# Kernel optimization log

Measured on AMD Instinct MI355X. Metric: run time of the kernel, lower is better.

The kernel has to match this reference:

```python
import jax, jax.numpy as jnp
import numpy as np
import math

N_NODES = 100000
N_EDGES = 1600000
CUTOFF = 6.0          # max_radius
NUM_RBF = 128         # ExpNormalSmearing num_rbf
GAUSS_MIN, GAUSS_MAX, GAUSS_NB = 0.0, 10.0, 32  # GaussianExpansion(0, 10, 32)


def setup_inputs() -> dict:
    key = jax.random.key(0)
    k1, k2 = jax.random.split(key)
    pos = jax.random.normal(k1, (N_NODES, 3), dtype=jnp.float32)
    edge_index = jax.random.randint(k2, (2, N_EDGES), 0, N_NODES, dtype=jnp.int64)
    return {"pos": pos, "edge_index": edge_index}


def _cosine_cutoff(d):
    # CosineCutoff with cutoff_lower=0
    c = 0.5 * (jnp.cos(d * (math.pi / CUTOFF)) + 1.0)
    return c * (d < CUTOFF).astype(d.dtype)


def _expnormal_smearing(d):
    # ExpNormalSmearing(cutoff_lower=0, cutoff_upper=CUTOFF, num_rbf=NUM_RBF)
    alpha = 5.0 / CUTOFF
    start = math.exp(-CUTOFF)
    means = jnp.linspace(start, 1.0, NUM_RBF, dtype=jnp.float32)
    beta = (2.0 / NUM_RBF * (1.0 - start)) ** (-2)
    d = d[:, None]                                   # [E,1]
    return _cosine_cutoff(d) * jnp.exp(-beta * (jnp.exp(-alpha * d) - means) ** 2)


def _gaussian_expansion(d):
    # GaussianExpansion(0, 10, 32)
    centers = jnp.linspace(GAUSS_MIN, GAUSS_MAX, GAUSS_NB, dtype=jnp.float32)
    width = 0.5 * (GAUSS_MAX - GAUSS_MIN) / GAUSS_NB
    d = d[:, None]
    return jnp.exp(-((d - centers) ** 2) / (2.0 * width * width))


def reference(pos, edge_index):
    src = edge_index[0]
    dst = edge_index[1]
    vec = pos[src] - pos[dst]                        # [E,3] irregular gather
    dist = jnp.sqrt(jnp.sum(vec * vec, axis=-1) + 1e-12)  # [E]
    exp_feat = _expnormal_smearing(dist)             # [E,128]
    gauss_feat = _gaussian_expansion(dist)           # [E,32]
    return jnp.concatenate([exp_feat, gauss_feat], axis=-1)  # [E,160]
```

## Files before the change

kernel.cpp:

```cpp
#include <hip/hip_runtime.h>
#include <math.h>

#define N_NODES   100000
#define N_EDGES   1600000
#define NUM_RBF   128
#define NUM_GAUSS 32
#define NFEAT     160
#define CUTOFF    6.0f

#define EPB    64
#define BLOCK  320
#define COLS   40
#define EPI    (BLOCK/COLS)
#define NITER  (EPB/EPI)

static __device__ __forceinline__ float fast_exp2(float x) {
#if __has_builtin(__builtin_amdgcn_exp2f)
    return __builtin_amdgcn_exp2f(x);
#else
    return __expf(0.6931471805599453f * x);
#endif
}

__global__ __launch_bounds__(BLOCK) void edge_feat_kernel(
    const float* __restrict__ pos,
    const int*   __restrict__ eidx,
    float*       __restrict__ out)
{
    __shared__ float4 s_edge[EPB];

    const int blockEdge0 = blockIdx.x * EPB;
    const int tid = threadIdx.x;

    if (tid < EPB) {
        const int e = blockEdge0 + tid;
        const int s = eidx[e];
        const int t = eidx[N_EDGES + e];
        const float dx = pos[3*s + 0] - pos[3*t + 0];
        const float dy = pos[3*s + 1] - pos[3*t + 1];
        const float dz = pos[3*s + 2] - pos[3*t + 2];
        const float dist = sqrtf(dx*dx + dy*dy + dz*dz + 1e-12f);
        const float c = 0.5f * (__cosf(dist * (float)(M_PI / 6.0)) + 1.0f);
        const float cc = (dist < CUTOFF) ? c : 0.0f;
        const float te = __expf(-(5.0f / 6.0f) * dist);
        s_edge[tid] = make_float4(dist, cc, te, 0.0f);
    }
    __syncthreads();

    const int col   = tid % COLS;
    const int eiter = tid / COLS;
    const bool isRBF = (col < NUM_RBF / 4);

    const float start = (float)0.0024787521766663585;
    const float mstep = (float)((1.0 - 0.0024787521766663585) / (NUM_RBF - 1));
    const float beta  = (float)(1.0 /
        ((2.0 / NUM_RBF * (1.0 - 0.0024787521766663585)) *
         (2.0 / NUM_RBF * (1.0 - 0.0024787521766663585))));
    const float gstep = (float)(10.0 / (NUM_GAUSS - 1));
    const float ginv  = 20.48f;
    const float LOG2E = 1.4426950408889634f;

    const int f0 = col * 4;
    float4 C;
    float SB;
    if (isRBF) {
        C.x = start + (float)(f0 + 0) * mstep;
        C.y = start + (float)(f0 + 1) * mstep;
        C.z = start + (float)(f0 + 2) * mstep;
        C.w = start + (float)(f0 + 3) * mstep;
        SB  = sqrtf(beta * LOG2E);
    } else {
        const int g0 = f0 - NUM_RBF;
        C.x = (float)(g0 + 0) * gstep;
        C.y = (float)(g0 + 1) * gstep;
        C.z = (float)(g0 + 2) * gstep;
        C.w = (float)(g0 + 3) * gstep;
        SB  = sqrtf(ginv * LOG2E);
    }

    float4* out4 = (float4*)(out + (size_t)blockEdge0 * NFEAT);
    #pragma unroll
    for (int k = 0; k < NITER; ++k) {
        const float4 es = s_edge[k * EPI + eiter];
        const float X = isRBF ? es.z : es.x;
        const float A = isRBF ? es.y : 1.0f;
        float4 r;
        {
            const float vx = (X - C.x) * SB;
            const float vy = (X - C.y) * SB;
            const float vz = (X - C.z) * SB;
            const float vw = (X - C.w) * SB;
            r.x = A * fast_exp2(-vx * vx);
            r.y = A * fast_exp2(-vy * vy);
            r.z = A * fast_exp2(-vz * vz);
            r.w = A * fast_exp2(-vw * vw);
        }
        out4[k * BLOCK + tid] = r;
    }
}

extern "C" void kernel_launch(void* const* d_in, const int* in_sizes, int n_in,
                              void* d_out, int out_size, void* d_ws, size_t ws_size,
                              hipStream_t stream) {
    const float* pos  = (const float*)d_in[0];
    const int*   eidx = (const int*)d_in[1];
    float*       out  = (float*)d_out;

    const int nblocks = N_EDGES / EPB;
    edge_feat_kernel<<<nblocks, BLOCK, 0, stream>>>(pos, eidx, out);
}
```

Baseline: 988.1 us.

## Use persistent blocks with double-buffered prefetch of next chunk's edge gathers

Turns the one-block-per-chunk launch into a persistent grid of 2500 blocks, each looping over 10 chunks of 64 edges. The index and position gathers for the next chunk are issued before the current chunk's features are computed and stored, and results go into a double-buffered shared array. The aim is to hide the irregular gather latency behind the output writes. In exchange there are fewer resident blocks to hide latency, extra registers, and a barrier on every iteration.

```diff
diff --git a/kernel.cpp b/kernel.cpp
--- a/kernel.cpp
+++ b/kernel.cpp
@@ -13,6 +13,8 @@
 #define COLS   40
 #define EPI    (BLOCK/COLS)
 #define NITER  (EPB/EPI)
+#define NCHUNK (N_EDGES/EPB)
+#define GRID   2500
 
 static __device__ __forceinline__ float fast_exp2(float x) {
 #if __has_builtin(__builtin_amdgcn_exp2f)
@@ -27,25 +29,10 @@
     const int*   __restrict__ eidx,
     float*       __restrict__ out)
 {
-    __shared__ float4 s_edge[EPB];
+    __shared__ float4 s_edge[2][EPB];
 
-    const int blockEdge0 = blockIdx.x * EPB;
     const int tid = threadIdx.x;
-
-    if (tid < EPB) {
-        const int e = blockEdge0 + tid;
-        const int s = eidx[e];
-        const int t = eidx[N_EDGES + e];
-        const float dx = pos[3*s + 0] - pos[3*t + 0];
-        const float dy = pos[3*s + 1] - pos[3*t + 1];
-        const float dz = pos[3*s + 2] - pos[3*t + 2];
-        const float dist = sqrtf(dx*dx + dy*dy + dz*dz + 1e-12f);
-        const float c = 0.5f * (__cosf(dist * (float)(M_PI / 6.0)) + 1.0f);
-        const float cc = (dist < CUTOFF) ? c : 0.0f;
-        const float te = __expf(-(5.0f / 6.0f) * dist);
-        s_edge[tid] = make_float4(dist, cc, te, 0.0f);
-    }
-    __syncthreads();
+    const bool writer = (tid < EPB);
 
     const int col   = tid % COLS;
     const int eiter = tid / COLS;
@@ -78,24 +65,70 @@
         SB  = sqrtf(ginv * LOG2E);
     }
 
-    float4* out4 = (float4*)(out + (size_t)blockEdge0 * NFEAT);
-    #pragma unroll
-    for (int k = 0; k < NITER; ++k) {
-        const float4 es = s_edge[k * EPI + eiter];
-        const float X = isRBF ? es.z : es.x;
-        const float A = isRBF ? es.y : 1.0f;
-        float4 r;
-        {
-            const float vx = (X - C.x) * SB;
-            const float vy = (X - C.y) * SB;
-            const float vz = (X - C.z) * SB;
-            const float vw = (X - C.w) * SB;
-            r.x = A * fast_exp2(-vx * vx);
-            r.y = A * fast_exp2(-vy * vy);
-            r.z = A * fast_exp2(-vz * vz);
-            r.w = A * fast_exp2(-vw * vw);
+    int c = blockIdx.x;
+    if (writer) {
+        const int e = c * EPB + tid;
+        const int s = eidx[e];
+        const int t = eidx[N_EDGES + e];
+        const float dx = pos[3*s + 0] - pos[3*t + 0];
+        const float dy = pos[3*s + 1] - pos[3*t + 1];
+        const float dz = pos[3*s + 2] - pos[3*t + 2];
+        const float dist = sqrtf(dx*dx + dy*dy + dz*dz + 1e-12f);
+        const float cth = 0.5f * (__cosf(dist * (float)(M_PI / 6.0)) + 1.0f);
+        const float cc = (dist < CUTOFF) ? cth : 0.0f;
+        const float te = __expf(-(5.0f / 6.0f) * dist);
+        s_edge[0][tid] = make_float4(dist, cc, te, 0.0f);
+    }
+    __syncthreads();
+
+    int buf = 0;
+    for (; c < NCHUNK; c += GRID) {
+        const int  cn  = c + GRID;
+        const bool pre = writer && (cn < NCHUNK);
+
+        int   sA = 0, tA = 0;
+        float ax = 0.f, ay = 0.f, az = 0.f, bx = 0.f, by = 0.f, bz = 0.f;
+        if (pre) {
+            const int e = cn * EPB + tid;
+            sA = eidx[e];
+            tA = eidx[N_EDGES + e];
+            ax = pos[3*sA + 0]; ay = pos[3*sA + 1]; az = pos[3*sA + 2];
+            bx = pos[3*tA + 0]; by = pos[3*tA + 1]; bz = pos[3*tA + 2];
         }
-        out4[k * BLOCK + tid] = r;
+
+        float4* out4 = (float4*)(out + (size_t)c * EPB * NFEAT);
+        #pragma unroll
+        for (int k = 0; k < NITER; ++k) {
+            const float4 es = s_edge[buf][k * EPI + eiter];
+            const float X = isRBF ? es.z : es.x;
+            const float A = isRBF ? es.y : 1.0f;
+            float4 r;
+            {
+                const float vx = (X - C.x) * SB;
+                const float vy = (X - C.y) * SB;
+                const float vz = (X - C.z) * SB;
+                const float vw = (X - C.w) * SB;
+                r.x = A * fast_exp2(-vx * vx);
+                r.y = A * fast_exp2(-vy * vy);
+                r.z = A * fast_exp2(-vz * vz);
+                r.w = A * fast_exp2(-vw * vw);
+            }
+            out4[k * BLOCK + tid] = r;
+        }
+
+        if (pre) {
+            const float dx = ax - bx;
+            const float dy = ay - by;
+            const float dz = az - bz;
+            const float dist = sqrtf(dx*dx + dy*dy + dz*dz + 1e-12f);
+            const float cth = 0.5f * (__cosf(dist * (float)(M_PI / 6.0)) + 1.0f);
+            const float cc = (dist < CUTOFF) ? cth : 0.0f;
+            const float te = __expf(-(5.0f / 6.0f) * dist);
+            s_edge[buf ^ 1][tid] = make_float4(dist, cc, te, 0.0f);
+        }
+
+        __syncthreads();
+        buf ^= 1;
     }
 }
 
@@ -106,6 +139,5 @@
     const int*   eidx = (const int*)d_in[1];
     float*       out  = (float*)d_out;
 
-    const int nblocks = N_EDGES / EPB;
-    edge_feat_kernel<<<nblocks, BLOCK, 0, stream>>>(pos, eidx, out);
+    edge_feat_kernel<<<GRID, BLOCK, 0, stream>>>(pos, eidx, out);
 }
```

Result: slower. 1.009 ms (+2.1%).

## Replace shared-memory edge staging with grid-stride per-thread recomputation

Applied to the files above, without the earlier changes.

Removes the shared-memory staging and block barrier. Each thread now gathers positions and computes the distance, cutoff and exponential for its own edge inside a grid-stride loop with a fixed grid of persistent blocks. The goal is to let the irregular gathers overlap with the output stores instead of stalling a block at the barrier. In exchange, each edge's gather and transcendental math is repeated by all 40 threads that handle it.

```diff
diff --git a/kernel.cpp b/kernel.cpp
--- a/kernel.cpp
+++ b/kernel.cpp
@@ -8,11 +8,11 @@
 #define NFEAT     160
 #define CUTOFF    6.0f
 
-#define EPB    64
-#define BLOCK  320
 #define COLS   40
-#define EPI    (BLOCK/COLS)
-#define NITER  (EPB/EPI)
+#define BLOCK  256
+#define GRID   2080
+#define STRIDE (GRID * BLOCK)
+#define ESTRIDE (STRIDE / COLS)
 
 static __device__ __forceinline__ float fast_exp2(float x) {
 #if __has_builtin(__builtin_amdgcn_exp2f)
@@ -27,28 +27,8 @@
     const int*   __restrict__ eidx,
     float*       __restrict__ out)
 {
-    __shared__ float4 s_edge[EPB];
-
-    const int blockEdge0 = blockIdx.x * EPB;
-    const int tid = threadIdx.x;
-
-    if (tid < EPB) {
-        const int e = blockEdge0 + tid;
-        const int s = eidx[e];
-        const int t = eidx[N_EDGES + e];
-        const float dx = pos[3*s + 0] - pos[3*t + 0];
-        const float dy = pos[3*s + 1] - pos[3*t + 1];
-        const float dz = pos[3*s + 2] - pos[3*t + 2];
-        const float dist = sqrtf(dx*dx + dy*dy + dz*dz + 1e-12f);
-        const float c = 0.5f * (__cosf(dist * (float)(M_PI / 6.0)) + 1.0f);
-        const float cc = (dist < CUTOFF) ? c : 0.0f;
-        const float te = __expf(-(5.0f / 6.0f) * dist);
-        s_edge[tid] = make_float4(dist, cc, te, 0.0f);
-    }
-    __syncthreads();
-
-    const int col   = tid % COLS;
-    const int eiter = tid / COLS;
+    const int g0  = blockIdx.x * BLOCK + threadIdx.x;
+    const int col = g0 % COLS;
     const bool isRBF = (col < NUM_RBF / 4);
 
     const float start = (float)0.0024787521766663585;
@@ -70,20 +50,33 @@
         C.w = start + (float)(f0 + 3) * mstep;
         SB  = sqrtf(beta * LOG2E);
     } else {
-        const int g0 = f0 - NUM_RBF;
-        C.x = (float)(g0 + 0) * gstep;
-        C.y = (float)(g0 + 1) * gstep;
-        C.z = (float)(g0 + 2) * gstep;
-        C.w = (float)(g0 + 3) * gstep;
+        const int g0f = f0 - NUM_RBF;
+        C.x = (float)(g0f + 0) * gstep;
+        C.y = (float)(g0f + 1) * gstep;
+        C.z = (float)(g0f + 2) * gstep;
+        C.w = (float)(g0f + 3) * gstep;
         SB  = sqrtf(ginv * LOG2E);
     }
 
-    float4* out4 = (float4*)(out + (size_t)blockEdge0 * NFEAT);
-    #pragma unroll
-    for (int k = 0; k < NITER; ++k) {
-        const float4 es = s_edge[k * EPI + eiter];
-        const float X = isRBF ? es.z : es.x;
-        const float A = isRBF ? es.y : 1.0f;
+    const size_t NF4 = (size_t)N_EDGES * COLS;
+    float4* out4 = (float4*)out;
+
+    int e = g0 / COLS;
+    #pragma unroll 4
+    for (size_t g = (size_t)g0; g < NF4; g += STRIDE, e += ESTRIDE) {
+        const int s = eidx[e];
+        const int t = eidx[N_EDGES + e];
+        const float dx = pos[3*s + 0] - pos[3*t + 0];
+        const float dy = pos[3*s + 1] - pos[3*t + 1];
+        const float dz = pos[3*s + 2] - pos[3*t + 2];
+        const float dist = sqrtf(dx*dx + dy*dy + dz*dz + 1e-12f);
+        const float cth = 0.5f * (__cosf(dist * (float)(M_PI / 6.0)) + 1.0f);
+        const float cc = (dist < CUTOFF) ? cth : 0.0f;
+        const float te = __expf(-(5.0f / 6.0f) * dist);
+
+        const float X = isRBF ? te : dist;
+        const float A = isRBF ? cc : 1.0f;
+
         float4 r;
         {
             const float vx = (X - C.x) * SB;
@@ -95,7 +88,7 @@
             r.z = A * fast_exp2(-vz * vz);
             r.w = A * fast_exp2(-vw * vw);
         }
-        out4[k * BLOCK + tid] = r;
+        out4[g] = r;
     }
 }
 
@@ -106,6 +99,5 @@
     const int*   eidx = (const int*)d_in[1];
     float*       out  = (float*)d_out;
 
-    const int nblocks = N_EDGES / EPB;
-    edge_feat_kernel<<<nblocks, BLOCK, 0, stream>>>(pos, eidx, out);
+    edge_feat_kernel<<<GRID, BLOCK, 0, stream>>>(pos, eidx, out);
 }
```

Result: slower. 1.075 ms (+8.8%).
